# Performance work log

Measured on AMD Instinct MI355X. Metric: run time of the kernel, lower is better.

Reference implementation:

```python
import jax, jax.numpy as jnp
import numpy as np

FEATURE_IN = 4096
FEATURE_OUT = 4096
R = 16
ALPHA = 32.0


def setup_inputs() -> dict:
    key = jax.random.key(0)
    k_x, k_w, k_b, k_a = jax.random.split(key, 4)
    x = jax.random.normal(k_x, (4, 2048, FEATURE_IN), dtype=jnp.float32)
    # base linear (torch nn.Linear): weight [out, in], bias [out]
    bound = 1.0 / np.sqrt(FEATURE_IN)
    w = jax.random.uniform(k_w, (FEATURE_OUT, FEATURE_IN), dtype=jnp.float32, minval=-bound, maxval=bound)
    b = jax.random.uniform(k_b, (FEATURE_OUT,), dtype=jnp.float32, minval=-bound, maxval=bound)
    # lora_a: kaiming uniform over [feature_in, r]; lora_b: zeros -> use small randn so grads are nontrivial? No: faithful init is zeros, but zeros makes LoRA path trivially zero. Use kaiming for a, small random for b to exercise the math.
    gain = np.sqrt(2.0 / (1.0 + 5.0 ** 2))  # kaiming_uniform default a=sqrt(5)
    bound_a = gain * np.sqrt(3.0 / FEATURE_IN)
    lora_a = jax.random.uniform(k_a, (FEATURE_IN, R), dtype=jnp.float32, minval=-bound_a, maxval=bound_a)
    lora_b = jax.random.normal(jax.random.fold_in(key, 7), (R, FEATURE_OUT), dtype=jnp.float32) * 0.01
    return {"x": x, "w": w, "b": b, "lora_a": lora_a, "lora_b": lora_b}


def reference(x, w, b, lora_a, lora_b):
    # base linear: x @ W^T + b
    output1 = jnp.einsum('bsi,oi->bso', x, w) + b
    # faithful to source: materialize (A @ B) [feature_in, feature_out] first,
    # then x @ (A@B), scaled by alpha/r
    ab = jnp.matmul(lora_a, lora_b)  # [feature_in, feature_out]
    output2 = jnp.matmul(x, ab) * (ALPHA / R)
    return output2 + output1
```

## Files before the change

kernel.cpp:

```cpp
#include <hip/hip_runtime.h>
#include <cstdint>
#include <cstddef>

#define FEATURE_IN 4096
#define FEATURE_OUT 4096
#define RNK 16

typedef __bf16 bf16x8_t __attribute__((ext_vector_type(8)));
typedef __bf16 bf16x4_t __attribute__((ext_vector_type(4)));
typedef float f32x4_t __attribute__((ext_vector_type(4)));

#define CVT_BLOCKS 2048
#define CVT_TPB 256
#define CVT_THREADS (CVT_BLOCKS * CVT_TPB)
#define CVT_CHUNKS 16

__global__ __launch_bounds__(CVT_TPB) void convert_x(const float* __restrict__ x,
                                                     uint16_t* __restrict__ xb) {
    const int tg = blockIdx.x * CVT_TPB + threadIdx.x;
    const float4* xp = (const float4*)x;
    bf16x4_t* op = (bf16x4_t*)xb;
#pragma unroll
    for (int i = 0; i < CVT_CHUNKS; ++i) {
        const int idx = i * CVT_THREADS + tg;
        float4 v = xp[idx];
        bf16x4_t o;
        o[0] = (__bf16)v.x; o[1] = (__bf16)v.y; o[2] = (__bf16)v.z; o[3] = (__bf16)v.w;
        op[idx] = o;
    }
}

#define FW_KB 128
#define FW_NB 32
#define NFUSE 4096

__global__ __launch_bounds__(256) void fuse_w(const float* __restrict__ w,
                                              const float* __restrict__ la,
                                              const float* __restrict__ lb,
                                              uint16_t* __restrict__ wf) {
    __shared__ float las[FW_KB * RNK];
    __shared__ float lbs[RNK * FW_NB];

    const int tid = threadIdx.x;
    const int bid = blockIdx.x;
    const int kb = (bid & 31) * FW_KB;
    const int nb = (bid >> 5) * FW_NB;

    {
        const float4* src = (const float4*)(la + (size_t)kb * RNK);
        float4* dst = (float4*)las;
        dst[tid] = src[tid];
        dst[tid + 256] = src[tid + 256];
    }
#pragma unroll
    for (int f = tid; f < RNK * FW_NB; f += 256) {
        int r = f >> 5;
        int nl = f & 31;
        lbs[r * FW_NB + nl] = lb[(size_t)r * FEATURE_OUT + nb + nl];
    }
    __syncthreads();

    const int nl = tid >> 3;
    const int kq = tid & 7;

    f32x4_t bcol[4];
#pragma unroll
    for (int r4 = 0; r4 < 4; ++r4) {
        f32x4_t v;
#pragma unroll
        for (int j = 0; j < 4; ++j) v[j] = lbs[(r4 * 4 + j) * FW_NB + nl];
        bcol[r4] = v;
    }

    const f32x4_t* las4 = (const f32x4_t*)las;
    const float* wrow = w + (size_t)(nb + nl) * FEATURE_IN + kb + kq * 16;
    uint16_t* wfrow = wf + (size_t)(nb + nl) * FEATURE_IN + kb + kq * 16;

#pragma unroll
    for (int h = 0; h < 2; ++h) {
        float4 wv0 = ((const float4*)wrow)[h * 2 + 0];
        float4 wv1 = ((const float4*)wrow)[h * 2 + 1];
        float wfv[8] = {wv0.x, wv0.y, wv0.z, wv0.w, wv1.x, wv1.y, wv1.z, wv1.w};
        bf16x8_t o;
#pragma unroll
        for (int j = 0; j < 8; ++j) {
            const int k = kq * 16 + h * 8 + j;
            float s = 0.f;
#pragma unroll
            for (int rr = 0; rr < 4; ++rr) {
                const int r4 = (rr + kq) & 3;
                f32x4_t av = las4[k * 4 + r4];
                f32x4_t bv = bcol[r4];
                s += av[0] * bv[0] + av[1] * bv[1] + av[2] * bv[2] + av[3] * bv[3];
            }
            o[j] = (__bf16)(wfv[j] + 2.f * s);
        }
        ((bf16x8_t*)wfrow)[h] = o;
    }
}

#define BM 256
#define BN 256
#define BK 64
#define NT (FEATURE_IN / BK)

#define ABASE(P, KS) ((P) * 65536 + (KS) * 16384)
#define BBASE(P, KS) ((P) * 65536 + 32768 + (KS) * 16384)

#define READ_A(G, P, KS) do { _Pragma("unroll")                                          \
    for (int _mi = 0; _mi < 4; ++_mi)                                                    \
        a[_mi] = *(const bf16x8_t*)(lds + ABASE(P, KS) + aoff[(G) * 4 + _mi]); } while (0)

#define READ_B(P, KS) do { _Pragma("unroll")                                             \
    for (int _ni = 0; _ni < 4; ++_ni)                                                    \
        b[_ni] = *(const bf16x8_t*)(lds + BBASE(P, KS) + boff[_ni]); } while (0)

#define MFMA_G(G) do { _Pragma("unroll")                                                 \
    for (int _mi = 0; _mi < 4; ++_mi) { _Pragma("unroll")                                \
        for (int _ni = 0; _ni < 4; ++_ni)                                                \
            acc[(G) * 4 + _mi][_ni] = __builtin_amdgcn_mfma_f32_16x16x32_bf16(           \
                a[_mi], b[_ni], acc[(G) * 4 + _mi][_ni], 0, 0, 0); } } while (0)

#define STAGE_A(PN, KS) do {                                                             \
    __builtin_amdgcn_global_load_lds(                                                    \
        (const __attribute__((address_space(1))) void*)(pA0 + (KS) * 32),                \
        (__attribute__((address_space(3))) void*)(lds + ABASE(PN, KS) + wv * 1024),      \
        16, 0, 0);                                                                       \
    __builtin_amdgcn_global_load_lds(                                                    \
        (const __attribute__((address_space(1))) void*)(pA1 + (KS) * 32),                \
        (__attribute__((address_space(3))) void*)(lds + ABASE(PN, KS) + 8192 + wv * 1024),\
        16, 0, 0); } while (0)

#define STAGE_B(PN, KS) do {                                                             \
    __builtin_amdgcn_global_load_lds(                                                    \
        (const __attribute__((address_space(1))) void*)(pB0 + (KS) * 32),                \
        (__attribute__((address_space(3))) void*)(lds + BBASE(PN, KS) + wv * 1024),      \
        16, 0, 0);                                                                       \
    __builtin_amdgcn_global_load_lds(                                                    \
        (const __attribute__((address_space(1))) void*)(pB1 + (KS) * 32),                \
        (__attribute__((address_space(3))) void*)(lds + BBASE(PN, KS) + 8192 + wv * 1024),\
        16, 0, 0); } while (0)

#define PBAR() __builtin_amdgcn_s_barrier()
#define PRIO1 __builtin_amdgcn_s_setprio(1)
#define PRIO0 __builtin_amdgcn_s_setprio(0)
#define VMCNT(n) asm volatile("s_waitcnt vmcnt(" #n ")" ::: "memory")

#define TILE_BODY(P, PN)                                                                 \
                                                                            \
    READ_A(0, P, 0); READ_B(P, 0);                                                       \
    STAGE_A(PN, 0);                                                                      \
    PBAR();                                                                              \
    PRIO1; MFMA_G(0); PRIO0;                                                             \
    PBAR();                                                                              \
                                                                            \
    READ_A(1, P, 0);                                                                     \
    STAGE_B(PN, 0);                                                                      \
    PBAR();                                                                              \
    PRIO1; MFMA_G(1); PRIO0;                                                             \
    VMCNT(4);                                                                            \
    PBAR();                                                                              \
                                                                            \
    READ_A(0, P, 1); READ_B(P, 1);                                                       \
    STAGE_A(PN, 1);                                                                      \
    PBAR();                                                                              \
    PRIO1; MFMA_G(0); PRIO0;                                                             \
    PBAR();                                                                              \
                                                                            \
    READ_A(1, P, 1);                                                                     \
    STAGE_B(PN, 1);                                                                      \
    PBAR();                                                                              \
    PRIO1; MFMA_G(1); PRIO0;                                                             \
    VMCNT(4);                                                                            \
    PBAR();                                                                              \
    pA0 += BK; pA1 += BK; pB0 += BK; pB1 += BK;

__global__ __launch_bounds__(512, 2) void gemm256(const uint16_t* __restrict__ Au,
                                                  const uint16_t* __restrict__ Bu,
                                                  const float* __restrict__ bias,
                                                  float* __restrict__ C,
                                                  int M, int N, int K) {
    __shared__ __align__(16) char lds[131072];

    const __bf16* A = (const __bf16*)Au;
    const __bf16* B = (const __bf16*)Bu;

    const int tid  = threadIdx.x;
    const int wv   = tid >> 6;
    const int lane = tid & 63;
    const int waveM = wv >> 2;
    const int waveN = wv & 3;
    const int l15 = lane & 15;
    const int q   = lane >> 4;

    const int nbx = N / BN;
    const int nwg = nbx * (M / BM);
    const int bidlin = blockIdx.y * nbx + blockIdx.x;
    const int swz = (bidlin & 7) * (nwg >> 3) + (bidlin >> 3);
    const int by = swz / nbx;
    const int bx = swz - by * nbx;
    const int m0 = by * BM;
    const int n0 = bx * BN;

    const int srow = tid >> 2;
    const int sq   = ((tid & 3) - (srow >> 1)) & 3;
    const __bf16* pA0 = A + (size_t)(m0 + srow) * K + sq * 8;
    const __bf16* pA1 = pA0 + (size_t)128 * K;
    const __bf16* pB0 = B + (size_t)(n0 + srow) * K + sq * 8;
    const __bf16* pB1 = pB0 + (size_t)128 * K;

    int aoff[8], boff[4];
#pragma unroll
    for (int mi = 0; mi < 8; ++mi) {
        int row = waveM * 128 + mi * 16 + l15;
        aoff[mi] = row * 64 + (((row >> 1) + q) & 3) * 16;
    }
#pragma unroll
    for (int ni = 0; ni < 4; ++ni) {
        int row = waveN * 64 + ni * 16 + l15;
        boff[ni] = row * 64 + (((row >> 1) + q) & 3) * 16;
    }

    f32x4_t acc[8][4];
#pragma unroll
    for (int mi = 0; mi < 8; ++mi)
#pragma unroll
        for (int ni = 0; ni < 4; ++ni)
            acc[mi][ni] = (f32x4_t)0.f;

    bf16x8_t a[4], b[4];

    STAGE_A(0, 0); STAGE_B(0, 0); STAGE_A(0, 1); STAGE_B(0, 1);
    pA0 += BK; pA1 += BK; pB0 += BK; pB1 += BK;
    VMCNT(4);
    PBAR();

#pragma unroll 1
    for (int i = 0; i < (NT - 2) / 2; ++i) {
        TILE_BODY(0, 1)
        TILE_BODY(1, 0)
    }
    TILE_BODY(0, 1)

    READ_A(0, 1, 0); READ_B(1, 0);
    PRIO1; MFMA_G(0); PRIO0;
    READ_A(1, 1, 0);
    PRIO1; MFMA_G(1); PRIO0;
    VMCNT(0);
    PBAR();
    READ_A(0, 1, 1); READ_B(1, 1);
    PRIO1; MFMA_G(0); PRIO0;
    READ_A(1, 1, 1);
    PRIO1; MFMA_G(1); PRIO0;

#pragma unroll
    for (int ni = 0; ni < 4; ++ni) {
        const int col = n0 + waveN * 64 + ni * 16 + l15;
        const float bv = bias[col];
#pragma unroll
        for (int mi = 0; mi < 8; ++mi) {
            const int row = m0 + waveM * 128 + mi * 16 + q * 4;
            float* op = C + (size_t)row * N + col;
#pragma unroll
            for (int j = 0; j < 4; ++j)
                op[(size_t)j * N] = acc[mi][ni][j] + bv;
        }
    }
}

extern "C" void kernel_launch(void* const* d_in, const int* in_sizes, int n_in,
                              void* d_out, int out_size, void* d_ws, size_t ws_size,
                              hipStream_t stream) {
    const float* x  = (const float*)d_in[0];
    const float* w  = (const float*)d_in[1];
    const float* b  = (const float*)d_in[2];
    const float* la = (const float*)d_in[3];
    const float* lb = (const float*)d_in[4];
    float* out = (float*)d_out;

    const int M = in_sizes[0] / FEATURE_IN;
    const int K = FEATURE_IN;
    const int N = FEATURE_OUT;

    uint16_t* xb = (uint16_t*)d_ws;
    uint16_t* wf = (uint16_t*)((char*)d_ws + (size_t)M * K * 2);

    convert_x<<<CVT_BLOCKS, CVT_TPB, 0, stream>>>(x, xb);

    fuse_w<<<NFUSE, 256, 0, stream>>>(w, la, lb, wf);

    {
        dim3 grid(N / BN, M / BM);
        gemm256<<<grid, 512, 0, stream>>>(xb, wf, b, out, M, N, K);
    }
}
```

Before: 532.0 us.

## Merge prep kernels and deepen GEMM pipeline to four BK=32 LDS stages

Merges the x-conversion and weight-fusion kernels into one launch, with blocks split by index, to save a launch and let the two run concurrently. The GEMM main loop changes from a double-buffered BK=64 scheme (two k-substeps per buffer) to a four-stage ring of BK=32 buffers, with three tiles prefetched ahead and a vmcnt of 8. This is meant to hide global-load latency better while using the same LDS footprint. The cost is more barriers per unit of K and a more complex drain sequence.

Measured after the change: 513.6 us. 1.04x faster.

```diff
diff --git a/kernel.cpp b/kernel.cpp
--- a/kernel.cpp
+++ b/kernel.cpp
@@ -10,38 +10,39 @@
 typedef __bf16 bf16x4_t __attribute__((ext_vector_type(4)));
 typedef float f32x4_t __attribute__((ext_vector_type(4)));
 
-#define CVT_BLOCKS 2048
-#define CVT_TPB 256
-#define CVT_THREADS (CVT_BLOCKS * CVT_TPB)
-#define CVT_CHUNKS 16
-
-__global__ __launch_bounds__(CVT_TPB) void convert_x(const float* __restrict__ x,
-                                                     uint16_t* __restrict__ xb) {
-    const int tg = blockIdx.x * CVT_TPB + threadIdx.x;
-    const float4* xp = (const float4*)x;
-    bf16x4_t* op = (bf16x4_t*)xb;
-#pragma unroll
-    for (int i = 0; i < CVT_CHUNKS; ++i) {
-        const int idx = i * CVT_THREADS + tg;
-        float4 v = xp[idx];
-        bf16x4_t o;
-        o[0] = (__bf16)v.x; o[1] = (__bf16)v.y; o[2] = (__bf16)v.z; o[3] = (__bf16)v.w;
-        op[idx] = o;
-    }
-}
-
 #define FW_KB 128
 #define FW_NB 32
 #define NFUSE 4096
-
-__global__ __launch_bounds__(256) void fuse_w(const float* __restrict__ w,
-                                              const float* __restrict__ la,
-                                              const float* __restrict__ lb,
-                                              uint16_t* __restrict__ wf) {
+#define NCVTB 2048
+#define CVT_THREADS (NCVTB * 256)
+#define CVT_CHUNKS 16
+
+__global__ __launch_bounds__(256) void prep_all(const float* __restrict__ x,
+                                                uint16_t* __restrict__ xb,
+                                                const float* __restrict__ w,
+                                                const float* __restrict__ la,
+                                                const float* __restrict__ lb,
+                                                uint16_t* __restrict__ wf) {
     __shared__ float las[FW_KB * RNK];
     __shared__ float lbs[RNK * FW_NB];
 
     const int tid = threadIdx.x;
+
+    if (blockIdx.x >= NFUSE) {
+        const int tg = (blockIdx.x - NFUSE) * 256 + tid;
+        const float4* xp = (const float4*)x;
+        bf16x4_t* op = (bf16x4_t*)xb;
+#pragma unroll
+        for (int i = 0; i < CVT_CHUNKS; ++i) {
+            const int idx = i * CVT_THREADS + tg;
+            float4 v = xp[idx];
+            bf16x4_t o;
+            o[0] = (__bf16)v.x; o[1] = (__bf16)v.y; o[2] = (__bf16)v.z; o[3] = (__bf16)v.w;
+            op[idx] = o;
+        }
+        return;
+    }
+
     const int bid = blockIdx.x;
     const int kb = (bid & 31) * FW_KB;
     const int nb = (bid >> 5) * FW_NB;
@@ -101,79 +102,64 @@
 
 #define BM 256
 #define BN 256
-#define BK 64
+#define BK 32
 #define NT (FEATURE_IN / BK)
 
-#define ABASE(P, KS) ((P) * 65536 + (KS) * 16384)
-#define BBASE(P, KS) ((P) * 65536 + 32768 + (KS) * 16384)
-
-#define READ_A(G, P, KS) do { _Pragma("unroll")                                          \
+#define ABUF(b) ((b) * 32768)
+#define BBUF(b) ((b) * 32768 + 16384)
+
+#define READ_A0(b) do { _Pragma("unroll")                                                \
     for (int _mi = 0; _mi < 4; ++_mi)                                                    \
-        a[_mi] = *(const bf16x8_t*)(lds + ABASE(P, KS) + aoff[(G) * 4 + _mi]); } while (0)
-
-#define READ_B(P, KS) do { _Pragma("unroll")                                             \
+        af[_mi] = *(const bf16x8_t*)(lds + ABUF(b) + aoff[_mi]); } while (0)
+
+#define READ_A1(b) do { _Pragma("unroll")                                                \
+    for (int _mi = 0; _mi < 4; ++_mi)                                                    \
+        af[_mi] = *(const bf16x8_t*)(lds + ABUF(b) + aoff[4 + _mi]); } while (0)
+
+#define READ_B4(b) do { _Pragma("unroll")                                                \
     for (int _ni = 0; _ni < 4; ++_ni)                                                    \
-        b[_ni] = *(const bf16x8_t*)(lds + BBASE(P, KS) + boff[_ni]); } while (0)
-
-#define MFMA_G(G) do { _Pragma("unroll")                                                 \
+        bq[_ni] = *(const bf16x8_t*)(lds + BBUF(b) + boff[_ni]); } while (0)
+
+#define MFMA16(G) do { _Pragma("unroll")                                                 \
     for (int _mi = 0; _mi < 4; ++_mi) { _Pragma("unroll")                                \
         for (int _ni = 0; _ni < 4; ++_ni)                                                \
             acc[(G) * 4 + _mi][_ni] = __builtin_amdgcn_mfma_f32_16x16x32_bf16(           \
-                a[_mi], b[_ni], acc[(G) * 4 + _mi][_ni], 0, 0, 0); } } while (0)
-
-#define STAGE_A(PN, KS) do {                                                             \
+                af[_mi], bq[_ni], acc[(G) * 4 + _mi][_ni], 0, 0, 0); } } while (0)
+
+#define GLL(SRC, DSTOFF)                                                                 \
     __builtin_amdgcn_global_load_lds(                                                    \
-        (const __attribute__((address_space(1))) void*)(pA0 + (KS) * 32),                \
-        (__attribute__((address_space(3))) void*)(lds + ABASE(PN, KS) + wv * 1024),      \
-        16, 0, 0);                                                                       \
-    __builtin_amdgcn_global_load_lds(                                                    \
-        (const __attribute__((address_space(1))) void*)(pA1 + (KS) * 32),                \
-        (__attribute__((address_space(3))) void*)(lds + ABASE(PN, KS) + 8192 + wv * 1024),\
-        16, 0, 0); } while (0)
-
-#define STAGE_B(PN, KS) do {                                                             \
-    __builtin_amdgcn_global_load_lds(                                                    \
-        (const __attribute__((address_space(1))) void*)(pB0 + (KS) * 32),                \
-        (__attribute__((address_space(3))) void*)(lds + BBASE(PN, KS) + wv * 1024),      \
-        16, 0, 0);                                                                       \
-    __builtin_amdgcn_global_load_lds(                                                    \
-        (const __attribute__((address_space(1))) void*)(pB1 + (KS) * 32),                \
-        (__attribute__((address_space(3))) void*)(lds + BBASE(PN, KS) + 8192 + wv * 1024),\
-        16, 0, 0); } while (0)
+        (const __attribute__((address_space(1))) void*)(SRC),                            \
+        (__attribute__((address_space(3))) void*)(lds + (DSTOFF) + wv * 1024), 16, 0, 0)
+
+#define STAGE_A(b) do { GLL(pA0, ABUF(b)); GLL(pA1, ABUF(b) + 8192); } while (0)
+#define STAGE_B(b) do { GLL(pB0, BBUF(b)); GLL(pB1, BBUF(b) + 8192); } while (0)
 
 #define PBAR() __builtin_amdgcn_s_barrier()
 #define PRIO1 __builtin_amdgcn_s_setprio(1)
 #define PRIO0 __builtin_amdgcn_s_setprio(0)
 #define VMCNT(n) asm volatile("s_waitcnt vmcnt(" #n ")" ::: "memory")
 
-#define TILE_BODY(P, PN)                                                                 \
-                                                                            \
-    READ_A(0, P, 0); READ_B(P, 0);                                                       \
-    STAGE_A(PN, 0);                                                                      \
-    PBAR();                                                                              \
-    PRIO1; MFMA_G(0); PRIO0;                                                             \
-    PBAR();                                                                              \
-                                                                            \
-    READ_A(1, P, 0);                                                                     \
-    STAGE_B(PN, 0);                                                                      \
-    PBAR();                                                                              \
-    PRIO1; MFMA_G(1); PRIO0;                                                             \
-    VMCNT(4);                                                                            \
-    PBAR();                                                                              \
-                                                                            \
-    READ_A(0, P, 1); READ_B(P, 1);                                                       \
-    STAGE_A(PN, 1);                                                                      \
-    PBAR();                                                                              \
-    PRIO1; MFMA_G(0); PRIO0;                                                             \
-    PBAR();                                                                              \
-                                                                            \
-    READ_A(1, P, 1);                                                                     \
-    STAGE_B(PN, 1);                                                                      \
-    PBAR();                                                                              \
-    PRIO1; MFMA_G(1); PRIO0;                                                             \
-    VMCNT(4);                                                                            \
+#define TILE_BODY(CUR, NXT)                                                              \
+    READ_A0(CUR); READ_B4(CUR);                                                          \
+    STAGE_A(NXT);                                                                        \
+    PBAR();                                                                              \
+    PRIO1; MFMA16(0); PRIO0;                                                             \
+    PBAR();                                                                              \
+    READ_A1(CUR);                                                                        \
+    STAGE_B(NXT);                                                                        \
+    PBAR();                                                                              \
+    PRIO1; MFMA16(1); PRIO0;                                                             \
+    VMCNT(8);                                                                            \
     PBAR();                                                                              \
     pA0 += BK; pA1 += BK; pB0 += BK; pB1 += BK;
+
+#define DRAIN_BODY(CUR, NWAIT)                                                           \
+    READ_A0(CUR); READ_B4(CUR);                                                          \
+    PRIO1; MFMA16(0); PRIO0;                                                             \
+    READ_A1(CUR);                                                                        \
+    PRIO1; MFMA16(1); PRIO0;                                                             \
+    VMCNT(NWAIT);                                                                        \
+    PBAR();
 
 __global__ __launch_bounds__(512, 2) void gemm256(const uint16_t* __restrict__ Au,
                                                   const uint16_t* __restrict__ Bu,
@@ -228,30 +214,29 @@
         for (int ni = 0; ni < 4; ++ni)
             acc[mi][ni] = (f32x4_t)0.f;
 
-    bf16x8_t a[4], b[4];
-
-    STAGE_A(0, 0); STAGE_B(0, 0); STAGE_A(0, 1); STAGE_B(0, 1);
-    pA0 += BK; pA1 += BK; pB0 += BK; pB1 += BK;
-    VMCNT(4);
+    bf16x8_t af[4], bq[4];
+
+    STAGE_A(0); STAGE_B(0); pA0 += BK; pA1 += BK; pB0 += BK; pB1 += BK;
+    STAGE_A(1); STAGE_B(1); pA0 += BK; pA1 += BK; pB0 += BK; pB1 += BK;
+    STAGE_A(2); STAGE_B(2); pA0 += BK; pA1 += BK; pB0 += BK; pB1 += BK;
+    VMCNT(8);
     PBAR();
 
 #pragma unroll 1
-    for (int i = 0; i < (NT - 2) / 2; ++i) {
-        TILE_BODY(0, 1)
+    for (int i = 0; i < 31; ++i) {
+        TILE_BODY(0, 3)
         TILE_BODY(1, 0)
-    }
-    TILE_BODY(0, 1)
-
-    READ_A(0, 1, 0); READ_B(1, 0);
-    PRIO1; MFMA_G(0); PRIO0;
-    READ_A(1, 1, 0);
-    PRIO1; MFMA_G(1); PRIO0;
-    VMCNT(0);
-    PBAR();
-    READ_A(0, 1, 1); READ_B(1, 1);
-    PRIO1; MFMA_G(0); PRIO0;
-    READ_A(1, 1, 1);
-    PRIO1; MFMA_G(1); PRIO0;
+        TILE_BODY(2, 1)
+        TILE_BODY(3, 2)
+    }
+    TILE_BODY(0, 3)
+
+    DRAIN_BODY(1, 4)
+    DRAIN_BODY(2, 0)
+    READ_A0(3); READ_B4(3);
+    PRIO1; MFMA16(0); PRIO0;
+    READ_A1(3);
+    PRIO1; MFMA16(1); PRIO0;
 
 #pragma unroll
     for (int ni = 0; ni < 4; ++ni) {
@@ -285,9 +270,7 @@
     uint16_t* xb = (uint16_t*)d_ws;
     uint16_t* wf = (uint16_t*)((char*)d_ws + (size_t)M * K * 2);
 
-    convert_x<<<CVT_BLOCKS, CVT_TPB, 0, stream>>>(x, xb);
-
-    fuse_w<<<NFUSE, 256, 0, stream>>>(w, la, lb, wf);
+    prep_all<<<NFUSE + NCVTB, 256, 0, stream>>>(x, xb, w, la, lb, wf);
 
     {
         dim3 grid(N / BN, M / BM);
```
